# Kernel tuning notes

Hardware: AMD Instinct MI355X
Metric: run time of the kernel (lower is better)

Reference implementation:

```python
import jax, jax.numpy as jnp
import numpy as np

M = 30000          # number of internal octree nodes
N = 2              # branching factor per axis (N3Tree)
S = N ** 3         # children per node
D = 32             # data_dim
DEPTH_LIMIT = 10
MLP_RATIO = 2
L = 7 * M + 1      # number of leaf cells: 8*M - (M-1)


def _build_tree(seed=0):
    """Random recursive octree: parent_pack[i] = packed (parent_node,x,y,z) of node i."""
    rng = np.random.default_rng(seed)
    parent_pack = np.zeros(M, np.int32)
    node_depth = np.zeros(M, np.int32)
    occupied = np.zeros((M, S), bool)
    free = [(0, c) for c in range(S)]  # refinable cells (keeps child depth <= DEPTH_LIMIT-1)
    for i in range(1, M):
        j = int(rng.integers(len(free)))
        p, c = free[j]
        free[j] = free[-1]
        free.pop()
        occupied[p, c] = True
        parent_pack[i] = p * S + c
        node_depth[i] = node_depth[p] + 1
        if node_depth[i] <= DEPTH_LIMIT - 2:
            free.extend((i, c2) for c2 in range(S))
    leaf_idx = np.flatnonzero(~occupied.reshape(-1)).astype(np.int32)
    assert leaf_idx.shape[0] == L
    return parent_pack, node_depth, leaf_idx


def setup_inputs() -> dict:
    parent_pack, node_depth, leaf_idx = _build_tree()
    # torch.sort(parent_depth, dim=0, descending=True) sorts each column independently
    idx_sorted = np.sort(parent_pack)[::-1].copy()
    depth_sorted = np.sort(node_depth)[::-1].copy()
    key = jax.random.key(0)
    ks = jax.random.split(key, 8)
    H = D * MLP_RATIO
    return {
        "data": jax.random.normal(ks[0], (M, N, N, N, D), jnp.float32),
        "conv_w": jax.random.normal(ks[1], (DEPTH_LIMIT, D, D, S), jnp.float32) * 0.05,
        "conv_b": jnp.zeros((DEPTH_LIMIT, D), jnp.float32),
        "depth_weight": jnp.arange(1, DEPTH_LIMIT + 1, dtype=jnp.float32) / (DEPTH_LIMIT + 1),
        "hf_w1": jax.random.normal(ks[2], (D, H), jnp.float32) * 0.02,
        "hf_b1": jnp.zeros((H,), jnp.float32),
        "hf_w2": jax.random.normal(ks[3], (H, 3), jnp.float32) * 0.02,
        "hf_b2": jnp.zeros((3,), jnp.float32),
        "hs_w1": jax.random.normal(ks[4], (D, H), jnp.float32) * 0.02,
        "hs_b1": jnp.zeros((H,), jnp.float32),
        "hs_w2": jax.random.normal(ks[5], (H, 1), jnp.float32) * 0.02,
        "hs_b2": jnp.zeros((1,), jnp.float32),
        "idx_sorted": jnp.asarray(idx_sorted),
        "depth_sorted": jnp.asarray(depth_sorted),
        "node_depth": jnp.asarray(node_depth),
        "leaf_idx": jnp.asarray(leaf_idx),
    }


def _mlp(x, w1, b1, w2, b2):
    # timm Mlp (Linear-GELU-Drop-Linear-Drop), dropout is identity in eval
    return jax.nn.gelu(x @ w1 + b1, approximate=False) @ w2 + b2


def reference(data, conv_w, conv_b, depth_weight,
              hf_w1, hf_b1, hf_w2, hf_b2,
              hs_w1, hs_b1, hs_w2, hs_b2,
              idx_sorted, depth_sorted, node_depth, leaf_idx):
    Dd = data.shape[-1]

    def step(carry, inp):
        dat, feats = carry
        idx, dsort = inp
        p = idx // S
        cell = idx % S
        x, y, z = cell // (N * N), (cell // N) % N, cell % N
        blk = dat[p].reshape(S, Dd)            # [(N1 N2 N3), D]
        cd = node_depth[p]                     # conv chosen by node's own depth entry
        # TreeConv over the 8-cell block: y[o] = sum_{i,k} W[o,i,k] * x[i,k] + b[o]
        feat = jnp.einsum('oik,ki->o', conv_w[cd], blk) + conv_b[cd]
        dat = dat.at[p, x, y, z].set(feat)     # recursive scatter write into tree.data
        feats = feats + depth_weight[dsort] * feat
        return (dat, feats), None

    (data, feats), _ = jax.lax.scan(
        step, (data, jnp.zeros((Dd,), data.dtype)), (idx_sorted, depth_sorted))

    leaves = data.reshape(-1, Dd)[leaf_idx] + feats   # tree[:] + features, [L, D]
    f = _mlp(leaves, hf_w1, hf_b1, hf_w2, hf_b2)      # [L, 3]
    sigma = _mlp(leaves, hs_w1, hs_b1, hs_w2, hs_b2)  # [L, 1]
    return jnp.concatenate([f, sigma], axis=1)        # [L, 4]
```

## Files before the change

### kernel.cpp

```cpp
#include <hip/hip_runtime.h>
#include <hip/hip_bf16.h>
#include <math.h>


typedef __attribute__((ext_vector_type(8))) short short8;
typedef __attribute__((ext_vector_type(4))) float f32x4;

#define WT_N 81920
#define RCAP 30720
#define RSTRIDE 32
#define FSLOTS 256

__device__ __forceinline__ unsigned short f2bf(float x) {
    __hip_bfloat16 h = __float2bfloat16(x);
    return *reinterpret_cast<unsigned short*>(&h);
}
__device__ __forceinline__ float bf2f(unsigned short h) {
    union { float f; unsigned u; } v; v.u = ((unsigned)h) << 16;
    return v.f;
}

__device__ __forceinline__ float4 shfl4(float4 v, int src) {
    float4 r;
    r.x = __shfl(v.x, src, 64);
    r.y = __shfl(v.y, src, 64);
    r.z = __shfl(v.z, src, 64);
    r.w = __shfl(v.w, src, 64);
    return r;
}

__device__ __forceinline__ void red_ig(float4& T) {
    #pragma unroll
    for (int m = 8; m <= 32; m <<= 1) {
        T.x += __shfl_xor(T.x, m, 64);
        T.y += __shfl_xor(T.y, m, 64);
        T.z += __shfl_xor(T.z, m, 64);
        T.w += __shfl_xor(T.w, m, 64);
    }
}

__device__ __forceinline__ float gelu_fast(float x)
{
    float e = __expf(-1.702f * x);
    return x * __builtin_amdgcn_rcpf(1.0f + e);
}

__global__ __launch_bounds__(256) void zero_kernel(int* __restrict__ dst)
{
    int i = blockIdx.x * 256 + threadIdx.x;
    if (i < 10 * RSTRIDE) dst[i] = 0;
}

__global__ __launch_bounds__(256) void prep_kernel(
    const float* __restrict__ conv_w, float* __restrict__ Wt,
    const float* __restrict__ hf_w1, const float* __restrict__ hs_w1,
    short* __restrict__ bph, short* __restrict__ bpl,
    const int* __restrict__ idx_sorted, const int* __restrict__ node_depth,
    int* __restrict__ gcnt, int2* __restrict__ runlist,
    float* __restrict__ feats_part, int M)
{
    __shared__ float tl[32 * 257];
    __shared__ int hcnt[16], hbase[16];

    if (blockIdx.x < 10) {
        int d = blockIdx.x;
        int base = d * 8192;
        for (int t = threadIdx.x; t < 8192; t += 256)
            tl[(t >> 8) * 257 + (t & 255)] = conv_w[base + t];
        __syncthreads();
        for (int t = threadIdx.x; t < 8192; t += 256) {
            int o = t & 31, i = (t >> 5) & 31, k = t >> 10;
            Wt[base + t] = tl[o * 257 + i * 8 + k];
        }
        return;
    }

    if (threadIdx.x < 16) hcnt[threadIdx.x] = 0;
    __syncthreads();

    int j = (blockIdx.x - 10) * 256 + threadIdx.x;
    bool start = false;
    int d = 0, myp = 0, mypos = 0;

    if (j < M) {
        int p = idx_sorted[j] >> 3;
        start = (j == 0) || ((idx_sorted[j - 1] >> 3) != p);
        if (start) {
            d = node_depth[p];
            myp = p;
            mypos = atomicAdd(&hcnt[d], 1);
        }
    } else if (j < M + 512) {
        int jj = j - M;
        int lane = jj & 63;
        int q = jj >> 6;
        int m = q >> 2, tq = q & 3;
        int kg = lane >> 4, n0 = lane & 15, k0 = kg * 8;
        const float* __restrict__ w1 = m ? hs_w1 : hf_w1;
        #pragma unroll
        for (int i = 0; i < 8; ++i) {
            float w = w1[(k0 + i) * 64 + tq * 16 + n0];
            unsigned short hh = f2bf(w);
            bph[(q * 64 + lane) * 8 + i] = (short)hh;
            bpl[(q * 64 + lane) * 8 + i] = (short)f2bf(w - bf2f(hh));
        }
    } else if (j < M + 512 + FSLOTS * 32) {
        feats_part[j - (M + 512)] = 0.0f;
    }

    __syncthreads();
    if (threadIdx.x < 16) {
        int c = hcnt[threadIdx.x];
        if (c > 0) hbase[threadIdx.x] = atomicAdd(&gcnt[threadIdx.x * RSTRIDE], c);
    }
    __syncthreads();
    if (start) runlist[d * RCAP + hbase[d] + mypos] = make_int2(j, myp);
}

__device__ __forceinline__ void run_steps(
    float4& T, float4& blk, float4& pfs, int ec, float edw, int base16,
    int n, int p, bool valid, const float* __restrict__ W, float4 bias,
    int og, int og8, int ig, float* __restrict__ patch)
{
    if (!valid) return;
    int c = __shfl(ec, base16, 64);
    float4 wc0 = *(const float4*)(W + (c * 32 + ig * 4 + 0) * 32 + og);
    float4 wc1 = *(const float4*)(W + (c * 32 + ig * 4 + 1) * 32 + og);
    float4 wc2 = *(const float4*)(W + (c * 32 + ig * 4 + 2) * 32 + og);
    float4 wc3 = *(const float4*)(W + (c * 32 + ig * 4 + 3) * 32 + og);

    for (int s = 0;; ++s) {
        float dw = __shfl(edw, base16 + s, 64);
        float4 feat = {T.x + bias.x, T.y + bias.y, T.z + bias.z, T.w + bias.w};
        pfs.x = fmaf(dw, feat.x, pfs.x); pfs.y = fmaf(dw, feat.y, pfs.y);
        pfs.z = fmaf(dw, feat.z, pfs.z); pfs.w = fmaf(dw, feat.w, pfs.w);

        if (s + 1 == n) {
            if (p == 0 && c == 0 && ig == 0)
                *(float4*)(patch + og) = feat;
            return;
        }

        int cn = __shfl(ec, base16 + s + 1, 64);
        float4 nw0 = *(const float4*)(W + (cn * 32 + ig * 4 + 0) * 32 + og);
        float4 nw1 = *(const float4*)(W + (cn * 32 + ig * 4 + 1) * 32 + og);
        float4 nw2 = *(const float4*)(W + (cn * 32 + ig * 4 + 2) * 32 + og);
        float4 nw3 = *(const float4*)(W + (cn * 32 + ig * 4 + 3) * 32 + og);

        float4 ov = shfl4(blk, c * 8 + og8);
        float4 du = {feat.x - ov.x, feat.y - ov.y, feat.z - ov.z, feat.w - ov.w};
        if (ig == c) blk = feat;
        float4 u = shfl4(du, og8 * 8 + ig);

        float4 a4;
        a4.x = u.x * wc0.x; a4.y = u.x * wc0.y;
        a4.z = u.x * wc0.z; a4.w = u.x * wc0.w;
        a4.x = fmaf(u.y, wc1.x, a4.x); a4.y = fmaf(u.y, wc1.y, a4.y);
        a4.z = fmaf(u.y, wc1.z, a4.z); a4.w = fmaf(u.y, wc1.w, a4.w);
        a4.x = fmaf(u.z, wc2.x, a4.x); a4.y = fmaf(u.z, wc2.y, a4.y);
        a4.z = fmaf(u.z, wc2.z, a4.z); a4.w = fmaf(u.z, wc2.w, a4.w);
        a4.x = fmaf(u.w, wc3.x, a4.x); a4.y = fmaf(u.w, wc3.y, a4.y);
        a4.z = fmaf(u.w, wc3.z, a4.z); a4.w = fmaf(u.w, wc3.w, a4.w);
        red_ig(a4);
        T.x += a4.x; T.y += a4.y; T.z += a4.z; T.w += a4.w;

        c = cn;
        wc0 = nw0; wc1 = nw1; wc2 = nw2; wc3 = nw3;
    }
}

#define FMA16(T, X) \
    T.x = fmaf(X.x, w0.x, T.x); T.y = fmaf(X.x, w0.y, T.y); \
    T.z = fmaf(X.x, w0.z, T.z); T.w = fmaf(X.x, w0.w, T.w); \
    T.x = fmaf(X.y, w1.x, T.x); T.y = fmaf(X.y, w1.y, T.y); \
    T.z = fmaf(X.y, w1.z, T.z); T.w = fmaf(X.y, w1.w, T.w); \
    T.x = fmaf(X.z, w2.x, T.x); T.y = fmaf(X.z, w2.y, T.y); \
    T.z = fmaf(X.z, w2.z, T.z); T.w = fmaf(X.z, w2.w, T.w); \
    T.x = fmaf(X.w, w3.x, T.x); T.y = fmaf(X.w, w3.y, T.y); \
    T.z = fmaf(X.w, w3.z, T.z); T.w = fmaf(X.w, w3.w, T.w);

__global__ __launch_bounds__(256, 4) void conv_scan(
    const float* __restrict__ data, const float* __restrict__ Wt,
    const float* __restrict__ conv_b, const float* __restrict__ depth_weight,
    const int* __restrict__ idx_sorted, const int* __restrict__ depth_sorted,
    const int* __restrict__ gcnt, const int2* __restrict__ runlist,
    float* __restrict__ feats_part, float* __restrict__ patch, int M)
{
    __shared__ float fred[4][32];

    int w = (blockIdx.x * 256 + threadIdx.x) >> 6;
    int l = threadIdx.x & 63;
    int wv = threadIdx.x >> 6;
    int og8 = l & 7, og = og8 * 4, ig = l >> 3;
    int q = l >> 4;

    int acc = 0, d = -1, chunk = 0, cnt = 0;
    #pragma unroll
    for (int dd = 0; dd < 10; ++dd) {
        int c = gcnt[dd * RSTRIDE];
        int nw = (c + 3) >> 2;
        if (d < 0 && w < acc + nw) { d = dd; chunk = w - acc; cnt = c; }
        acc += nw;
    }

    float4 pfs = {0, 0, 0, 0};
    if (d >= 0) {
        int r0 = chunk * 4;
        int rq = r0 + q; if (rq >= cnt) rq = cnt - 1;
        int2 e = runlist[d * RCAP + rq];
        int t0l = e.x, pl = e.y;

        int wl = l & 15;
        int tw = t0l + wl;
        int twc = tw < M ? tw : M - 1;
        int iw  = idx_sorted[twc];
        int dsw = depth_sorted[twc];
        unsigned long long mask = __ballot((tw < M) && ((iw >> 3) == pl));
        int   ec  = iw & 7;
        float edw = depth_weight[dsw & 15];

        const float* __restrict__ W = Wt + d * 8192;
        const float4 bias = *(const float4*)(conv_b + d * 32 + og);

        int p0 = __shfl(pl, 0, 64),  p1 = __shfl(pl, 16, 64),
            p2 = __shfl(pl, 32, 64), p3 = __shfl(pl, 48, 64);
        int n0 = __builtin_ctz(~(unsigned)( mask        & 0xFFFFull));
        int n1 = __builtin_ctz(~(unsigned)((mask >> 16) & 0xFFFFull));
        int n2 = __builtin_ctz(~(unsigned)((mask >> 32) & 0xFFFFull));
        int n3 = __builtin_ctz(~(unsigned)((mask >> 48) & 0xFFFFull));
        bool v0 = (r0 + 0 < cnt), v1 = (r0 + 1 < cnt),
             v2 = (r0 + 2 < cnt), v3 = (r0 + 3 < cnt);

        float4 B0 = *(const float4*)(data + (size_t)p0 * 256 + ig * 32 + og);
        float4 B1 = *(const float4*)(data + (size_t)p1 * 256 + ig * 32 + og);
        float4 B2 = *(const float4*)(data + (size_t)p2 * 256 + ig * 32 + og);
        float4 B3 = *(const float4*)(data + (size_t)p3 * 256 + ig * 32 + og);

        float4 T0 = {0,0,0,0}, T1 = {0,0,0,0}, T2 = {0,0,0,0}, T3 = {0,0,0,0};
        #pragma unroll
        for (int k = 0; k < 8; ++k) {
            const float4 w0 = *(const float4*)(W + (k * 32 + ig * 4 + 0) * 32 + og);
            const float4 w1 = *(const float4*)(W + (k * 32 + ig * 4 + 1) * 32 + og);
            const float4 w2 = *(const float4*)(W + (k * 32 + ig * 4 + 2) * 32 + og);
            const float4 w3 = *(const float4*)(W + (k * 32 + ig * 4 + 3) * 32 + og);
            int src = k * 8 + ig;
            float4 x0 = shfl4(B0, src), x1 = shfl4(B1, src),
                   x2 = shfl4(B2, src), x3 = shfl4(B3, src);
            FMA16(T0, x0); FMA16(T1, x1); FMA16(T2, x2); FMA16(T3, x3);
        }
        red_ig(T0); red_ig(T1); red_ig(T2); red_ig(T3);

        run_steps(T0, B0, pfs, ec, edw,  0, n0, p0, v0, W, bias, og, og8, ig, patch);
        run_steps(T1, B1, pfs, ec, edw, 16, n1, p1, v1, W, bias, og, og8, ig, patch);
        run_steps(T2, B2, pfs, ec, edw, 32, n2, p2, v2, W, bias, og, og8, ig, patch);
        run_steps(T3, B3, pfs, ec, edw, 48, n3, p3, v3, W, bias, og, og8, ig, patch);
    }

    if (ig == 0) {
        fred[wv][og + 0] = pfs.x;
        fred[wv][og + 1] = pfs.y;
        fred[wv][og + 2] = pfs.z;
        fred[wv][og + 3] = pfs.w;
    }
    __syncthreads();
    if (threadIdx.x < 32) {
        float s = fred[0][threadIdx.x] + fred[1][threadIdx.x]
                + fred[2][threadIdx.x] + fred[3][threadIdx.x];
        atomicAdd(&feats_part[(blockIdx.x & (FSLOTS - 1)) * 32 + threadIdx.x], s);
    }
}

__global__ __launch_bounds__(256, 4) void mlp_kernel(
    const float* __restrict__ data, const float* __restrict__ feats_part,
    const float* __restrict__ patch, const int* __restrict__ leaf_idx,
    const short* __restrict__ bph, const short* __restrict__ bpl,
    const float* __restrict__ hf_w1, const float* __restrict__ hs_w1,
    const float* __restrict__ hf_b1, const float* __restrict__ hf_w2,
    const float* __restrict__ hf_b2, const float* __restrict__ hs_b1,
    const float* __restrict__ hs_w2, const float* __restrict__ hs_b2,
    float* __restrict__ out, int L)
{
    __shared__ float red[256];
    __shared__ float sh_fts[32];
    __shared__ float sh_fvec[128];
    __shared__ __align__(16) short sh_b[4096];

    {
        int ch = threadIdx.x & 31, g = threadIdx.x >> 5;
        float s = 0.f;
        #pragma unroll
        for (int j = 0; j < FSLOTS / 8; ++j)
            s += feats_part[(g + j * 8) * 32 + ch];
        red[threadIdx.x] = s;
        __syncthreads();
        if (threadIdx.x < 128) red[threadIdx.x] += red[threadIdx.x + 128];
        __syncthreads();
        if (threadIdx.x < 64) red[threadIdx.x] += red[threadIdx.x + 64];
        __syncthreads();
        if (threadIdx.x < 32)
            sh_fts[threadIdx.x] = red[threadIdx.x] + red[threadIdx.x + 32];
        __syncthreads();
    }

    {
        const int4* src = (const int4*)bph;
        int4* dst = (int4*)sh_b;
        for (int t = threadIdx.x; t < 512; t += 256) dst[t] = src[t];

        if (threadIdx.x < 128) {
            int m = threadIdx.x >> 6, h = threadIdx.x & 63;
            const float* __restrict__ w1 = m ? hs_w1 : hf_w1;
            float s = 0.f;
            #pragma unroll
            for (int k = 0; k < 32; ++k) s = fmaf(sh_fts[k], w1[k * 64 + h], s);
            sh_fvec[threadIdx.x] = s;
        }
        __syncthreads();
    }

    int l = threadIdx.x & 63;
    int ck = blockIdx.x * 4 + (threadIdx.x >> 6);
    int nchunks = (L + 63) >> 6;
    if (ck >= nchunks) return;
    int base = ck * 64;
    int n0 = l & 15, kg = l >> 4, k0 = kg * 8;

    float w2r[16], b1r[8];
    #pragma unroll
    for (int t = 0; t < 4; ++t) {
        int h = t * 16 + n0;
        w2r[t * 4 + 0] = hf_w2[h * 3 + 0];
        w2r[t * 4 + 1] = hf_w2[h * 3 + 1];
        w2r[t * 4 + 2] = hf_w2[h * 3 + 2];
        w2r[t * 4 + 3] = hs_w2[h];
        b1r[t]     = hf_b1[h] + sh_fvec[h];
        b1r[4 + t] = hs_b1[h] + sh_fvec[64 + h];
    }
    float b20 = hf_b2[0], b21 = hf_b2[1], b22 = hf_b2[2], b23 = hs_b2[0];

    #pragma unroll
    for (int tm = 0; tm < 4; ++tm) {
        int r  = base + tm * 16 + n0;
        int rc = r < L ? r : L - 1;
        int row = leaf_idx[rc];
        const float* __restrict__ src = (row == 0) ? patch : (data + (size_t)row * 32);
        float4 vA = *(const float4*)(src + k0);
        float4 vB = *(const float4*)(src + k0 + 4);
        float xv[8] = {vA.x, vA.y, vA.z, vA.w, vB.x, vB.y, vB.z, vB.w};
        short8 ahi;
        #pragma unroll
        for (int i = 0; i < 8; ++i) ahi[i] = (short)f2bf(xv[i]);

        f32x4 acc[8];
        bool anyPatch = __any(row == 0);
        if (!anyPatch) {
            #pragma unroll
            for (int qq = 0; qq < 8; ++qq) {
                short8 bh = *(const short8*)(sh_b + (qq * 64 + l) * 8);
                float bv = b1r[qq];
                f32x4 a = (f32x4){bv, bv, bv, bv};
                acc[qq] = __builtin_amdgcn_mfma_f32_16x16x32_bf16(ahi, bh, a, 0, 0, 0);
            }
        } else {
            short8 alo;
            #pragma unroll
            for (int i = 0; i < 8; ++i) {
                unsigned short hh = (unsigned short)ahi[i];
                alo[i] = (short)f2bf(xv[i] - bf2f(hh));
            }
            #pragma unroll
            for (int qq = 0; qq < 8; ++qq) {
                short8 bh = *(const short8*)(sh_b + (qq * 64 + l) * 8);
                short8 bl = *(const short8*)(bpl + (qq * 64 + l) * 8);
                float bv = b1r[qq];
                f32x4 a = (f32x4){bv, bv, bv, bv};
                a = __builtin_amdgcn_mfma_f32_16x16x32_bf16(ahi, bh, a, 0, 0, 0);
                a = __builtin_amdgcn_mfma_f32_16x16x32_bf16(alo, bh, a, 0, 0, 0);
                a = __builtin_amdgcn_mfma_f32_16x16x32_bf16(ahi, bl, a, 0, 0, 0);
                acc[qq] = a;
            }
        }

        float o[4][4];
        #pragma unroll
        for (int g2 = 0; g2 < 4; ++g2) {
            #pragma unroll
            for (int c = 0; c < 4; ++c) o[g2][c] = 0.f;
        }
        #pragma unroll
        for (int t = 0; t < 4; ++t) {
            #pragma unroll
            for (int reg = 0; reg < 4; ++reg) {
                float gf = gelu_fast(acc[t][reg]);
                float gs = gelu_fast(acc[4 + t][reg]);
                o[reg][0] = fmaf(gf, w2r[t * 4 + 0], o[reg][0]);
                o[reg][1] = fmaf(gf, w2r[t * 4 + 1], o[reg][1]);
                o[reg][2] = fmaf(gf, w2r[t * 4 + 2], o[reg][2]);
                o[reg][3] = fmaf(gs, w2r[t * 4 + 3], o[reg][3]);
            }
        }
        #pragma unroll
        for (int mk = 1; mk < 16; mk <<= 1) {
            #pragma unroll
            for (int reg = 0; reg < 4; ++reg) {
                #pragma unroll
                for (int c = 0; c < 4; ++c)
                    o[reg][c] += __shfl_xor(o[reg][c], mk, 64);
            }
        }
        if (n0 < 4) {
            int rL = base + tm * 16 + kg * 4 + n0;
            if (rL < L) {
                float s0 = n0 == 0 ? o[0][0] : n0 == 1 ? o[1][0] : n0 == 2 ? o[2][0] : o[3][0];
                float s1 = n0 == 0 ? o[0][1] : n0 == 1 ? o[1][1] : n0 == 2 ? o[2][1] : o[3][1];
                float s2 = n0 == 0 ? o[0][2] : n0 == 1 ? o[1][2] : n0 == 2 ? o[2][2] : o[3][2];
                float s3 = n0 == 0 ? o[0][3] : n0 == 1 ? o[1][3] : n0 == 2 ? o[2][3] : o[3][3];
                float4 res = {s0 + b20, s1 + b21, s2 + b22, s3 + b23};
                *(float4*)(out + (size_t)rL * 4) = res;
            }
        }
    }
}

extern "C" void kernel_launch(void* const* d_in, const int* in_sizes, int n_in,
                              void* d_out, int out_size, void* d_ws, size_t ws_size,
                              hipStream_t stream)
{
    const float* data         = (const float*)d_in[0];
    const float* conv_w       = (const float*)d_in[1];
    const float* conv_b       = (const float*)d_in[2];
    const float* depth_weight = (const float*)d_in[3];
    const float* hf_w1        = (const float*)d_in[4];
    const float* hf_b1        = (const float*)d_in[5];
    const float* hf_w2        = (const float*)d_in[6];
    const float* hf_b2        = (const float*)d_in[7];
    const float* hs_w1        = (const float*)d_in[8];
    const float* hs_b1        = (const float*)d_in[9];
    const float* hs_w2        = (const float*)d_in[10];
    const float* hs_b2        = (const float*)d_in[11];
    const int*   idx_sorted   = (const int*)d_in[12];
    const int*   depth_sorted = (const int*)d_in[13];
    const int*   node_depth   = (const int*)d_in[14];
    const int*   leaf_idx     = (const int*)d_in[15];

    int M = in_sizes[12];
    int L = in_sizes[15];
    float* out = (float*)d_out;

    float* Wt         = (float*)d_ws;
    float* patch      = Wt + WT_N;
    short* bph        = (short*)(patch + 32);
    short* bpl        = bph + 4096;
    int*   gcnt       = (int*)(bpl + 4096);
    float* feats_part = (float*)(gcnt + 10 * RSTRIDE);
    int2*  runlist    = (int2*)(feats_part + FSLOTS * 32);

    zero_kernel<<<2, 256, 0, stream>>>(gcnt);

    int nb_prep = 10 + (M + 512 + FSLOTS * 32 + 255) / 256;
    prep_kernel<<<nb_prep, 256, 0, stream>>>(
        conv_w, Wt, hf_w1, hs_w1, bph, bpl,
        idx_sorted, node_depth, gcnt, runlist, feats_part, M);

    int max_waves = (M + 3) / 4 + 10;
    conv_scan<<<(max_waves + 3) / 4, 256, 0, stream>>>(
        data, Wt, conv_b, depth_weight, idx_sorted, depth_sorted,
        gcnt, runlist, feats_part, patch, M);

    int nchunks = (L + 63) / 64;
    mlp_kernel<<<(nchunks + 3) / 4, 256, 0, stream>>>(
        data, feats_part, patch, leaf_idx, bph, bpl,
        hf_w1, hs_w1,
        hf_b1, hf_w2, hf_b2, hs_b1, hs_w2, hs_b2, out, L);
}
```

Before: 58.33 us.

## Stage per-depth conv weights in swizzled LDS and assign blocks per depth

Each conv_scan block is now assigned to a single depth and covers 16 runs (4 per wave). The block first copies that depth's 32 KB weight slab into shared memory with an XOR swizzle, then all waves read weights from LDS instead of issuing repeated global/L1 loads. The aim is to cut redundant weight fetches from cache, since four waves now share one copy. The cost is a 32 KB LDS footprint per block that may limit occupancy, a barrier before compute, and partially idle waves in each depth's last block.

```diff
diff --git a/kernel.cpp b/kernel.cpp
--- a/kernel.cpp
+++ b/kernel.cpp
@@ -45,6 +45,11 @@
     return x * __builtin_amdgcn_rcpf(1.0f + e);
 }
 
+__device__ __forceinline__ float4 ldsW4(const float4* tlW, int row, int og8) {
+    int g = row * 8 + og8;
+    return tlW[g ^ ((g >> 5) & 7)];
+}
+
 __global__ __launch_bounds__(256) void zero_kernel(int* __restrict__ dst)
 {
     int i = blockIdx.x * 256 + threadIdx.x;
@@ -119,15 +124,15 @@
 
 __device__ __forceinline__ void run_steps(
     float4& T, float4& blk, float4& pfs, int ec, float edw, int base16,
-    int n, int p, bool valid, const float* __restrict__ W, float4 bias,
+    int n, int p, bool valid, const float4* tlW, float4 bias,
     int og, int og8, int ig, float* __restrict__ patch)
 {
     if (!valid) return;
     int c = __shfl(ec, base16, 64);
-    float4 wc0 = *(const float4*)(W + (c * 32 + ig * 4 + 0) * 32 + og);
-    float4 wc1 = *(const float4*)(W + (c * 32 + ig * 4 + 1) * 32 + og);
-    float4 wc2 = *(const float4*)(W + (c * 32 + ig * 4 + 2) * 32 + og);
-    float4 wc3 = *(const float4*)(W + (c * 32 + ig * 4 + 3) * 32 + og);
+    float4 wc0 = ldsW4(tlW, c * 32 + ig * 4 + 0, og8);
+    float4 wc1 = ldsW4(tlW, c * 32 + ig * 4 + 1, og8);
+    float4 wc2 = ldsW4(tlW, c * 32 + ig * 4 + 2, og8);
+    float4 wc3 = ldsW4(tlW, c * 32 + ig * 4 + 3, og8);
 
     for (int s = 0;; ++s) {
         float dw = __shfl(edw, base16 + s, 64);
@@ -142,10 +147,10 @@
         }
 
         int cn = __shfl(ec, base16 + s + 1, 64);
-        float4 nw0 = *(const float4*)(W + (cn * 32 + ig * 4 + 0) * 32 + og);
-        float4 nw1 = *(const float4*)(W + (cn * 32 + ig * 4 + 1) * 32 + og);
-        float4 nw2 = *(const float4*)(W + (cn * 32 + ig * 4 + 2) * 32 + og);
-        float4 nw3 = *(const float4*)(W + (cn * 32 + ig * 4 + 3) * 32 + og);
+        float4 nw0 = ldsW4(tlW, cn * 32 + ig * 4 + 0, og8);
+        float4 nw1 = ldsW4(tlW, cn * 32 + ig * 4 + 1, og8);
+        float4 nw2 = ldsW4(tlW, cn * 32 + ig * 4 + 2, og8);
+        float4 nw3 = ldsW4(tlW, cn * 32 + ig * 4 + 3, og8);
 
         float4 ov = shfl4(blk, c * 8 + og8);
         float4 du = {feat.x - ov.x, feat.y - ov.y, feat.z - ov.z, feat.w - ov.w};
@@ -186,26 +191,37 @@
     const int* __restrict__ gcnt, const int2* __restrict__ runlist,
     float* __restrict__ feats_part, float* __restrict__ patch, int M)
 {
+    __shared__ __align__(16) float4 tlW[2048];
     __shared__ float fred[4][32];
 
-    int w = (blockIdx.x * 256 + threadIdx.x) >> 6;
+    int acc = 0, d = -1, chunk = 0, cnt = 0;
+    #pragma unroll
+    for (int dd = 0; dd < 10; ++dd) {
+        int c = gcnt[dd * RSTRIDE];
+        int nb = (c + 15) >> 4;
+        if (d < 0 && (int)blockIdx.x < acc + nb) {
+            d = dd; chunk = (int)blockIdx.x - acc; cnt = c;
+        }
+        acc += nb;
+    }
+    if (d < 0) return;
+
+    {
+        const float4* Wg = (const float4*)(Wt + d * 8192);
+        for (int g = threadIdx.x; g < 2048; g += 256)
+            tlW[g ^ ((g >> 5) & 7)] = Wg[g];
+    }
+    __syncthreads();
+
     int l = threadIdx.x & 63;
     int wv = threadIdx.x >> 6;
     int og8 = l & 7, og = og8 * 4, ig = l >> 3;
     int q = l >> 4;
 
-    int acc = 0, d = -1, chunk = 0, cnt = 0;
-    #pragma unroll
-    for (int dd = 0; dd < 10; ++dd) {
-        int c = gcnt[dd * RSTRIDE];
-        int nw = (c + 3) >> 2;
-        if (d < 0 && w < acc + nw) { d = dd; chunk = w - acc; cnt = c; }
-        acc += nw;
-    }
-
+    int r0 = chunk * 16 + wv * 4;
     float4 pfs = {0, 0, 0, 0};
-    if (d >= 0) {
-        int r0 = chunk * 4;
+
+    if (r0 < cnt) {
         int rq = r0 + q; if (rq >= cnt) rq = cnt - 1;
         int2 e = runlist[d * RCAP + rq];
         int t0l = e.x, pl = e.y;
@@ -219,7 +235,6 @@
         int   ec  = iw & 7;
         float edw = depth_weight[dsw & 15];
 
-        const float* __restrict__ W = Wt + d * 8192;
         const float4 bias = *(const float4*)(conv_b + d * 32 + og);
 
         int p0 = __shfl(pl, 0, 64),  p1 = __shfl(pl, 16, 64),
@@ -239,10 +254,10 @@
         float4 T0 = {0,0,0,0}, T1 = {0,0,0,0}, T2 = {0,0,0,0}, T3 = {0,0,0,0};
         #pragma unroll
         for (int k = 0; k < 8; ++k) {
-            const float4 w0 = *(const float4*)(W + (k * 32 + ig * 4 + 0) * 32 + og);
-            const float4 w1 = *(const float4*)(W + (k * 32 + ig * 4 + 1) * 32 + og);
-            const float4 w2 = *(const float4*)(W + (k * 32 + ig * 4 + 2) * 32 + og);
-            const float4 w3 = *(const float4*)(W + (k * 32 + ig * 4 + 3) * 32 + og);
+            const float4 w0 = ldsW4(tlW, k * 32 + ig * 4 + 0, og8);
+            const float4 w1 = ldsW4(tlW, k * 32 + ig * 4 + 1, og8);
+            const float4 w2 = ldsW4(tlW, k * 32 + ig * 4 + 2, og8);
+            const float4 w3 = ldsW4(tlW, k * 32 + ig * 4 + 3, og8);
             int src = k * 8 + ig;
             float4 x0 = shfl4(B0, src), x1 = shfl4(B1, src),
                    x2 = shfl4(B2, src), x3 = shfl4(B3, src);
@@ -250,10 +265,10 @@
         }
         red_ig(T0); red_ig(T1); red_ig(T2); red_ig(T3);
 
-        run_steps(T0, B0, pfs, ec, edw,  0, n0, p0, v0, W, bias, og, og8, ig, patch);
-        run_steps(T1, B1, pfs, ec, edw, 16, n1, p1, v1, W, bias, og, og8, ig, patch);
-        run_steps(T2, B2, pfs, ec, edw, 32, n2, p2, v2, W, bias, og, og8, ig, patch);
-        run_steps(T3, B3, pfs, ec, edw, 48, n3, p3, v3, W, bias, og, og8, ig, patch);
+        run_steps(T0, B0, pfs, ec, edw,  0, n0, p0, v0, tlW, bias, og, og8, ig, patch);
+        run_steps(T1, B1, pfs, ec, edw, 16, n1, p1, v1, tlW, bias, og, og8, ig, patch);
+        run_steps(T2, B2, pfs, ec, edw, 32, n2, p2, v2, tlW, bias, og, og8, ig, patch);
+        run_steps(T3, B3, pfs, ec, edw, 48, n3, p3, v3, tlW, bias, og, og8, ig, patch);
     }
 
     if (ig == 0) {
@@ -462,8 +477,8 @@
         conv_w, Wt, hf_w1, hs_w1, bph, bpl,
         idx_sorted, node_depth, gcnt, runlist, feats_part, M);
 
-    int max_waves = (M + 3) / 4 + 10;
-    conv_scan<<<(max_waves + 3) / 4, 256, 0, stream>>>(
+    int nb_conv = (M + 15) / 16 + 10;
+    conv_scan<<<nb_conv, 256, 0, stream>>>(
         data, Wt, conv_b, depth_weight, idx_sorted, depth_sorted,
         gcnt, runlist, feats_part, patch, M);
 
```

Result: slower. 62.98 us (+8.0%).

## Process four runs concurrently per wave using a 4x4 lane tiling in conv_scan

Applied to the files above, without the earlier changes.

The conv scan kernel is reorganized so each 16-lane quarter of a wave handles its own run of same-parent steps in parallel. Previously the four runs in a wave were walked one after another. Each lane now owns an 8-output by 8-input tile, loads block data straight from global memory instead of broadcasting it by shuffles, and reduces over only 4 lanes per step. The aim is to shorten the serial dependency chain and cut cross-lane shuffle traffic. In exchange, every lane issues more weight loads, quarters with shorter runs sit idle until the longest run finishes, and launch bounds rise to 8 waves per SIMD, which adds register pressure.

```diff
diff --git a/kernel.cpp b/kernel.cpp
--- a/kernel.cpp
+++ b/kernel.cpp
@@ -29,13 +29,23 @@
     return r;
 }
 
-__device__ __forceinline__ void red_ig(float4& T) {
+__device__ __forceinline__ void red_ig4(float4& A, float4& B) {
     #pragma unroll
-    for (int m = 8; m <= 32; m <<= 1) {
-        T.x += __shfl_xor(T.x, m, 64);
-        T.y += __shfl_xor(T.y, m, 64);
-        T.z += __shfl_xor(T.z, m, 64);
-        T.w += __shfl_xor(T.w, m, 64);
+    for (int m = 1; m <= 2; m <<= 1) {
+        A.x += __shfl_xor(A.x, m, 64); A.y += __shfl_xor(A.y, m, 64);
+        A.z += __shfl_xor(A.z, m, 64); A.w += __shfl_xor(A.w, m, 64);
+        B.x += __shfl_xor(B.x, m, 64); B.y += __shfl_xor(B.y, m, 64);
+        B.z += __shfl_xor(B.z, m, 64); B.w += __shfl_xor(B.w, m, 64);
+    }
+}
+
+__device__ __forceinline__ void red_q(float4& A, float4& B) {
+    #pragma unroll
+    for (int m = 16; m <= 32; m <<= 1) {
+        A.x += __shfl_xor(A.x, m, 64); A.y += __shfl_xor(A.y, m, 64);
+        A.z += __shfl_xor(A.z, m, 64); A.w += __shfl_xor(A.w, m, 64);
+        B.x += __shfl_xor(B.x, m, 64); B.y += __shfl_xor(B.y, m, 64);
+        B.z += __shfl_xor(B.z, m, 64); B.w += __shfl_xor(B.w, m, 64);
     }
 }
 
@@ -117,69 +127,13 @@
     if (start) runlist[d * RCAP + hbase[d] + mypos] = make_int2(j, myp);
 }
 
-__device__ __forceinline__ void run_steps(
-    float4& T, float4& blk, float4& pfs, int ec, float edw, int base16,
-    int n, int p, bool valid, const float* __restrict__ W, float4 bias,
-    int og, int og8, int ig, float* __restrict__ patch)
-{
-    if (!valid) return;
-    int c = __shfl(ec, base16, 64);
-    float4 wc0 = *(const float4*)(W + (c * 32 + ig * 4 + 0) * 32 + og);
-    float4 wc1 = *(const float4*)(W + (c * 32 + ig * 4 + 1) * 32 + og);
-    float4 wc2 = *(const float4*)(W + (c * 32 + ig * 4 + 2) * 32 + og);
-    float4 wc3 = *(const float4*)(W + (c * 32 + ig * 4 + 3) * 32 + og);
-
-    for (int s = 0;; ++s) {
-        float dw = __shfl(edw, base16 + s, 64);
-        float4 feat = {T.x + bias.x, T.y + bias.y, T.z + bias.z, T.w + bias.w};
-        pfs.x = fmaf(dw, feat.x, pfs.x); pfs.y = fmaf(dw, feat.y, pfs.y);
-        pfs.z = fmaf(dw, feat.z, pfs.z); pfs.w = fmaf(dw, feat.w, pfs.w);
-
-        if (s + 1 == n) {
-            if (p == 0 && c == 0 && ig == 0)
-                *(float4*)(patch + og) = feat;
-            return;
-        }
-
-        int cn = __shfl(ec, base16 + s + 1, 64);
-        float4 nw0 = *(const float4*)(W + (cn * 32 + ig * 4 + 0) * 32 + og);
-        float4 nw1 = *(const float4*)(W + (cn * 32 + ig * 4 + 1) * 32 + og);
-        float4 nw2 = *(const float4*)(W + (cn * 32 + ig * 4 + 2) * 32 + og);
-        float4 nw3 = *(const float4*)(W + (cn * 32 + ig * 4 + 3) * 32 + og);
-
-        float4 ov = shfl4(blk, c * 8 + og8);
-        float4 du = {feat.x - ov.x, feat.y - ov.y, feat.z - ov.z, feat.w - ov.w};
-        if (ig == c) blk = feat;
-        float4 u = shfl4(du, og8 * 8 + ig);
-
-        float4 a4;
-        a4.x = u.x * wc0.x; a4.y = u.x * wc0.y;
-        a4.z = u.x * wc0.z; a4.w = u.x * wc0.w;
-        a4.x = fmaf(u.y, wc1.x, a4.x); a4.y = fmaf(u.y, wc1.y, a4.y);
-        a4.z = fmaf(u.y, wc1.z, a4.z); a4.w = fmaf(u.y, wc1.w, a4.w);
-        a4.x = fmaf(u.z, wc2.x, a4.x); a4.y = fmaf(u.z, wc2.y, a4.y);
-        a4.z = fmaf(u.z, wc2.z, a4.z); a4.w = fmaf(u.z, wc2.w, a4.w);
-        a4.x = fmaf(u.w, wc3.x, a4.x); a4.y = fmaf(u.w, wc3.y, a4.y);
-        a4.z = fmaf(u.w, wc3.z, a4.z); a4.w = fmaf(u.w, wc3.w, a4.w);
-        red_ig(a4);
-        T.x += a4.x; T.y += a4.y; T.z += a4.z; T.w += a4.w;
-
-        c = cn;
-        wc0 = nw0; wc1 = nw1; wc2 = nw2; wc3 = nw3;
-    }
-}
-
-#define FMA16(T, X) \
-    T.x = fmaf(X.x, w0.x, T.x); T.y = fmaf(X.x, w0.y, T.y); \
-    T.z = fmaf(X.x, w0.z, T.z); T.w = fmaf(X.x, w0.w, T.w); \
-    T.x = fmaf(X.y, w1.x, T.x); T.y = fmaf(X.y, w1.y, T.y); \
-    T.z = fmaf(X.y, w1.z, T.z); T.w = fmaf(X.y, w1.w, T.w); \
-    T.x = fmaf(X.z, w2.x, T.x); T.y = fmaf(X.z, w2.y, T.y); \
-    T.z = fmaf(X.z, w2.z, T.z); T.w = fmaf(X.z, w2.w, T.w); \
-    T.x = fmaf(X.w, w3.x, T.x); T.y = fmaf(X.w, w3.y, T.y); \
-    T.z = fmaf(X.w, w3.z, T.z); T.w = fmaf(X.w, w3.w, T.w);
-
-__global__ __launch_bounds__(256, 4) void conv_scan(
+#define FMA8(TA, TB, X, WA, WB) \
+    TA.x = fmaf(X, WA.x, TA.x); TA.y = fmaf(X, WA.y, TA.y); \
+    TA.z = fmaf(X, WA.z, TA.z); TA.w = fmaf(X, WA.w, TA.w); \
+    TB.x = fmaf(X, WB.x, TB.x); TB.y = fmaf(X, WB.y, TB.y); \
+    TB.z = fmaf(X, WB.z, TB.z); TB.w = fmaf(X, WB.w, TB.w);
+
+__global__ __launch_bounds__(256, 8) void conv_scan(
     const float* __restrict__ data, const float* __restrict__ Wt,
     const float* __restrict__ conv_b, const float* __restrict__ depth_weight,
     const int* __restrict__ idx_sorted, const int* __restrict__ depth_sorted,
@@ -191,8 +145,11 @@
     int w = (blockIdx.x * 256 + threadIdx.x) >> 6;
     int l = threadIdx.x & 63;
     int wv = threadIdx.x >> 6;
-    int og8 = l & 7, og = og8 * 4, ig = l >> 3;
-    int q = l >> 4;
+    int lane16 = l & 15, q = l >> 4;
+    int og4 = lane16 >> 2, ig4 = lane16 & 3;
+    int ob = og4 * 8;
+    int ib = ig4 * 8;
+    int tsrc = (l & 48) | (ig4 << 2) | og4;
 
     int acc = 0, d = -1, chunk = 0, cnt = 0;
     #pragma unroll
@@ -203,64 +160,103 @@
         acc += nw;
     }
 
-    float4 pfs = {0, 0, 0, 0};
+    float4 pA = {0,0,0,0}, pB = {0,0,0,0};
     if (d >= 0) {
         int r0 = chunk * 4;
+        bool vq = (r0 + q < cnt);
         int rq = r0 + q; if (rq >= cnt) rq = cnt - 1;
         int2 e = runlist[d * RCAP + rq];
-        int t0l = e.x, pl = e.y;
-
-        int wl = l & 15;
-        int tw = t0l + wl;
+        int t0 = e.x, p = e.y;
+
+        int tw = t0 + lane16;
         int twc = tw < M ? tw : M - 1;
         int iw  = idx_sorted[twc];
         int dsw = depth_sorted[twc];
-        unsigned long long mask = __ballot((tw < M) && ((iw >> 3) == pl));
+        unsigned long long mask = __ballot((tw < M) && ((iw >> 3) == p));
+        int nq = __builtin_ctz(~(unsigned)((mask >> (q * 16)) & 0xFFFFull));
         int   ec  = iw & 7;
         float edw = depth_weight[dsw & 15];
 
         const float* __restrict__ W = Wt + d * 8192;
-        const float4 bias = *(const float4*)(conv_b + d * 32 + og);
-
-        int p0 = __shfl(pl, 0, 64),  p1 = __shfl(pl, 16, 64),
-            p2 = __shfl(pl, 32, 64), p3 = __shfl(pl, 48, 64);
-        int n0 = __builtin_ctz(~(unsigned)( mask        & 0xFFFFull));
-        int n1 = __builtin_ctz(~(unsigned)((mask >> 16) & 0xFFFFull));
-        int n2 = __builtin_ctz(~(unsigned)((mask >> 32) & 0xFFFFull));
-        int n3 = __builtin_ctz(~(unsigned)((mask >> 48) & 0xFFFFull));
-        bool v0 = (r0 + 0 < cnt), v1 = (r0 + 1 < cnt),
-             v2 = (r0 + 2 < cnt), v3 = (r0 + 3 < cnt);
-
-        float4 B0 = *(const float4*)(data + (size_t)p0 * 256 + ig * 32 + og);
-        float4 B1 = *(const float4*)(data + (size_t)p1 * 256 + ig * 32 + og);
-        float4 B2 = *(const float4*)(data + (size_t)p2 * 256 + ig * 32 + og);
-        float4 B3 = *(const float4*)(data + (size_t)p3 * 256 + ig * 32 + og);
-
-        float4 T0 = {0,0,0,0}, T1 = {0,0,0,0}, T2 = {0,0,0,0}, T3 = {0,0,0,0};
+        float4 biasA = *(const float4*)(conv_b + d * 32 + ob);
+        float4 biasB = *(const float4*)(conv_b + d * 32 + ob + 4);
+
+        float4 TA = {0,0,0,0}, TB = {0,0,0,0};
         #pragma unroll
         for (int k = 0; k < 8; ++k) {
-            const float4 w0 = *(const float4*)(W + (k * 32 + ig * 4 + 0) * 32 + og);
-            const float4 w1 = *(const float4*)(W + (k * 32 + ig * 4 + 1) * 32 + og);
-            const float4 w2 = *(const float4*)(W + (k * 32 + ig * 4 + 2) * 32 + og);
-            const float4 w3 = *(const float4*)(W + (k * 32 + ig * 4 + 3) * 32 + og);
-            int src = k * 8 + ig;
-            float4 x0 = shfl4(B0, src), x1 = shfl4(B1, src),
-                   x2 = shfl4(B2, src), x3 = shfl4(B3, src);
-            FMA16(T0, x0); FMA16(T1, x1); FMA16(T2, x2); FMA16(T3, x3);
-        }
-        red_ig(T0); red_ig(T1); red_ig(T2); red_ig(T3);
-
-        run_steps(T0, B0, pfs, ec, edw,  0, n0, p0, v0, W, bias, og, og8, ig, patch);
-        run_steps(T1, B1, pfs, ec, edw, 16, n1, p1, v1, W, bias, og, og8, ig, patch);
-        run_steps(T2, B2, pfs, ec, edw, 32, n2, p2, v2, W, bias, og, og8, ig, patch);
-        run_steps(T3, B3, pfs, ec, edw, 48, n3, p3, v3, W, bias, og, og8, ig, patch);
-    }
-
-    if (ig == 0) {
-        fred[wv][og + 0] = pfs.x;
-        fred[wv][og + 1] = pfs.y;
-        fred[wv][og + 2] = pfs.z;
-        fred[wv][og + 3] = pfs.w;
+            float4 xA = *(const float4*)(data + (size_t)p * 256 + k * 32 + ib);
+            float4 xB = *(const float4*)(data + (size_t)p * 256 + k * 32 + ib + 4);
+            #pragma unroll
+            for (int jj = 0; jj < 8; ++jj) {
+                float x = jj < 4 ? (jj == 0 ? xA.x : jj == 1 ? xA.y : jj == 2 ? xA.z : xA.w)
+                                 : (jj == 4 ? xB.x : jj == 5 ? xB.y : jj == 6 ? xB.z : xB.w);
+                const float4 wA = *(const float4*)(W + (k * 32 + ib + jj) * 32 + ob);
+                const float4 wB = *(const float4*)(W + (k * 32 + ib + jj) * 32 + ob + 4);
+                FMA8(TA, TB, x, wA, wB);
+            }
+        }
+        red_ig4(TA, TB);
+
+        int nn = vq ? nq : 0;
+        nn = max(nn, __shfl_xor(nn, 16, 64));
+        nn = max(nn, __shfl_xor(nn, 32, 64));
+        int nmax = nn;
+
+        int c = __shfl(ec, q * 16 + 0, 64);
+        int cprev = -1;
+        float4 fpA = {0,0,0,0}, fpB = {0,0,0,0};
+
+        for (int s = 0; s < nmax; ++s) {
+            bool act = vq && (s < nq);
+            float dw = __shfl(edw, q * 16 + s, 64);
+            float4 fA = {TA.x + biasA.x, TA.y + biasA.y, TA.z + biasA.z, TA.w + biasA.w};
+            float4 fB = {TB.x + biasB.x, TB.y + biasB.y, TB.z + biasB.z, TB.w + biasB.w};
+            float m = act ? dw : 0.f;
+            pA.x = fmaf(m, fA.x, pA.x); pA.y = fmaf(m, fA.y, pA.y);
+            pA.z = fmaf(m, fA.z, pA.z); pA.w = fmaf(m, fA.w, pA.w);
+            pB.x = fmaf(m, fB.x, pB.x); pB.y = fmaf(m, fB.y, pB.y);
+            pB.z = fmaf(m, fB.z, pB.z); pB.w = fmaf(m, fB.w, pB.w);
+
+            if (act && (s + 1 == nq) && p == 0 && c == 0 && ig4 == 0) {
+                *(float4*)(patch + ob) = fA;
+                *(float4*)(patch + ob + 4) = fB;
+            }
+
+            if (s + 1 < nmax) {
+                int cn = __shfl(ec, q * 16 + s + 1, 64);
+                float4 ovA, ovB;
+                if (c == cprev) { ovA = fpA; ovB = fpB; }
+                else {
+                    ovA = *(const float4*)(data + (size_t)p * 256 + c * 32 + ob);
+                    ovB = *(const float4*)(data + (size_t)p * 256 + c * 32 + ob + 4);
+                }
+                float4 duA = {fA.x - ovA.x, fA.y - ovA.y, fA.z - ovA.z, fA.w - ovA.w};
+                float4 duB = {fB.x - ovB.x, fB.y - ovB.y, fB.z - ovB.z, fB.w - ovB.w};
+                float4 uA = shfl4(duA, tsrc);
+                float4 uB = shfl4(duB, tsrc);
+
+                float4 aA = {0,0,0,0}, aB = {0,0,0,0};
+                #pragma unroll
+                for (int jj = 0; jj < 8; ++jj) {
+                    float x = jj < 4 ? (jj == 0 ? uA.x : jj == 1 ? uA.y : jj == 2 ? uA.z : uA.w)
+                                     : (jj == 4 ? uB.x : jj == 5 ? uB.y : jj == 6 ? uB.z : uB.w);
+                    const float4 wA = *(const float4*)(W + (c * 32 + ib + jj) * 32 + ob);
+                    const float4 wB = *(const float4*)(W + (c * 32 + ib + jj) * 32 + ob + 4);
+                    FMA8(aA, aB, x, wA, wB);
+                }
+                red_ig4(aA, aB);
+                TA.x += aA.x; TA.y += aA.y; TA.z += aA.z; TA.w += aA.w;
+                TB.x += aB.x; TB.y += aB.y; TB.z += aB.z; TB.w += aB.w;
+
+                fpA = fA; fpB = fB; cprev = c; c = cn;
+            }
+        }
+    }
+
+    red_q(pA, pB);
+    if (l < 16 && (l & 3) == 0) {
+        *(float4*)(&fred[wv][ob])     = pA;
+        *(float4*)(&fred[wv][ob + 4]) = pB;
     }
     __syncthreads();
     if (threadIdx.x < 32) {
```

After: 136.0 us. 133% more time.
